# Optimization experiments

Hardware: AMD Instinct MI355X
Metric: run time of the kernel (lower is better)

Reference implementation:

```python
import jax, jax.numpy as jnp
import numpy as np

N_NODES = 100000
N_EDGES = 1600000
N_GRAPHS = 64
HIDDEN = 128


def _gcn_conv(x, W, b, src, dst, norm, n_nodes):
    # PyG GCNConv: out_i = sum_{j->i} norm_ij * (x_j W) + b, with self-loops
    h = x @ W                                   # [N, out]
    msg = h[src] * norm[:, None]                # gather over edges (incl. self-loops)
    out = jax.ops.segment_sum(msg, dst, num_segments=n_nodes)
    return out + b


def _gcn_norm(src, dst, n_nodes):
    # add self-loops, symmetric normalization deg^-1/2 * deg^-1/2
    loops = jnp.arange(n_nodes, dtype=src.dtype)
    src_f = jnp.concatenate([src, loops])
    dst_f = jnp.concatenate([dst, loops])
    deg = jax.ops.segment_sum(jnp.ones_like(dst_f, dtype=jnp.float32), dst_f,
                              num_segments=n_nodes)
    dis = jnp.where(deg > 0, jax.lax.rsqrt(deg), 0.0)
    norm = dis[src_f] * dis[dst_f]
    return src_f, dst_f, norm


def setup_inputs() -> dict:
    key = jax.random.key(0)
    ks = jax.random.split(key, 8)
    x = jax.random.normal(ks[0], (N_NODES, 10), dtype=jnp.float32)
    edge_index = jax.random.randint(ks[1], (2, N_EDGES), 0, N_NODES, dtype=jnp.int64)
    batch = jnp.sort(jax.random.randint(ks[2], (N_NODES,), 0, N_GRAPHS, dtype=jnp.int64))
    g = lambda k, shape: jax.random.normal(k, shape, dtype=jnp.float32) * (1.0 / np.sqrt(shape[0]))
    return {
        "x": x, "edge_index": edge_index, "batch": batch,
        "W1": g(ks[3], (10, HIDDEN)), "b1": jnp.zeros((HIDDEN,), jnp.float32),
        "W2": g(ks[4], (HIDDEN, HIDDEN)), "b2": jnp.zeros((HIDDEN,), jnp.float32),
        "W3": g(ks[5], (HIDDEN, HIDDEN)), "b3": jnp.zeros((HIDDEN,), jnp.float32),
        "Wlin": g(ks[6], (HIDDEN, 3)), "blin": jnp.zeros((3,), jnp.float32),
    }


def reference(x, edge_index, batch, W1, b1, W2, b2, W3, b3, Wlin, blin):
    n = x.shape[0]
    src, dst, norm = _gcn_norm(edge_index[0], edge_index[1], n)
    h = jax.nn.relu(_gcn_conv(x, W1, b1, src, dst, norm, n))
    h = jax.nn.relu(_gcn_conv(h, W2, b2, src, dst, norm, n))
    h = _gcn_conv(h, W3, b3, src, dst, norm, n)
    # global mean pool over graphs
    sums = jax.ops.segment_sum(h, batch, num_segments=N_GRAPHS)
    cnts = jax.ops.segment_sum(jnp.ones((n,), jnp.float32), batch, num_segments=N_GRAPHS)
    pooled = sums / jnp.maximum(cnts, 1.0)[:, None]
    # dropout p=0.5 is identity at eval time
    return pooled @ Wlin + blin
```

## Files before the change

kernel.cpp:

```cpp
#include <hip/hip_runtime.h>

constexpr int NN = 100000;
constexpr int NE = 1600000;
constexpr int NG = 64;
constexpr int H  = 128;

constexpr int NB  = 392;
constexpr int CAP = 5120;
constexpr int P1B = 256;
constexpr int EPB = NE / P1B;

typedef float v2f   __attribute__((ext_vector_type(2)));
typedef float f32x4 __attribute__((ext_vector_type(4)));
typedef short short8 __attribute__((ext_vector_type(8)));

__device__ __forceinline__ float bf_lo(unsigned v) { return __uint_as_float(v << 16); }
__device__ __forceinline__ float bf_hi(unsigned v) { return __uint_as_float(v & 0xffff0000u); }
__device__ __forceinline__ unsigned bf_pack(float a, float b) {
  unsigned ua = __float_as_uint(a);
  unsigned ub = __float_as_uint(b);
  ua += 0x7fffu + ((ua >> 16) & 1u);
  ub += 0x7fffu + ((ub >> 16) & 1u);
  return (ua >> 16) | (ub & 0xffff0000u);
}
__device__ __forceinline__ ushort bf1(float a) {
  unsigned u = __float_as_uint(a);
  u += 0x7fffu + ((u >> 16) & 1u);
  return (ushort)(u >> 16);
}

__device__ __forceinline__ float swap32(float v) {
  int idx = (((int)threadIdx.x & 63) ^ 32) << 2;
  return __int_as_float(__builtin_amdgcn_ds_bpermute(idx, __float_as_int(v)));
}

__global__ void k_init(float* pool, float* cnt, int* gcursor) {
  int i = blockIdx.x * blockDim.x + threadIdx.x;
  if (i < NG * H) pool[i] = 0.f;
  if (i < NG) cnt[i] = 0.f;
  if (i < NB) gcursor[i] = i * CAP;
}

__global__ void k_bucket(const int* __restrict__ ei, int* __restrict__ gcursor,
                         unsigned* __restrict__ ebuf, int* __restrict__ dirs,
                         ushort* __restrict__ dirl) {
  __shared__ int cnt[NB];
  __shared__ int cpos[NB];
  int t = threadIdx.x, b = blockIdx.x;
  for (int j = t; j < NB; j += 256) cnt[j] = 0;
  __syncthreads();
  int e0 = b * EPB;
  for (int i = t; i < EPB; i += 256) {
    int d = ei[NE + e0 + i];
    atomicAdd(&cnt[d >> 8], 1);
  }
  __syncthreads();
  for (int j = t; j < NB; j += 256) {
    int c = cnt[j];
    int start = atomicAdd(&gcursor[j], c);
    cpos[j] = start;
    dirs[b * NB + j] = start;
    dirl[b * NB + j] = (ushort)c;
  }
  __syncthreads();
  for (int j = t; j < NB; j += 256) cnt[j] = 0;
  __syncthreads();
  for (int i = t; i < EPB; i += 256) {
    int s = ei[e0 + i];
    int d = ei[NE + e0 + i];
    int bk = d >> 8;
    int slot = cpos[bk] + atomicAdd(&cnt[bk], 1);
    ebuf[slot] = (unsigned)s | ((unsigned)(d & 255) << 17);
  }
}

__global__ void k_bucketscan(const int* __restrict__ gcursor, int* __restrict__ gbase,
                             int* __restrict__ offs) {
  if (threadIdx.x == 0) {
    int run = 0;
    for (int j = 0; j < NB; ++j) {
      int tot = gcursor[j] - j * CAP;
      gbase[j] = run; run += tot;
    }
    gbase[NB] = run;
    offs[NN] = run;
  }
}

__global__ void k_csr(const unsigned* __restrict__ ebuf, const int* __restrict__ dirs,
                      const ushort* __restrict__ dirl, const int* __restrict__ gbase,
                      const float* __restrict__ x,
                      int* __restrict__ offs, float* __restrict__ dis,
                      unsigned* __restrict__ xs16, int* __restrict__ csr, int n) {
  __shared__ int histc[256];
  __shared__ int loffs[256];
  __shared__ int wps[4];
  int t = threadIdx.x, j = blockIdx.x;
  histc[t] = 0;
  __syncthreads();
  int cstart = dirs[t * NB + j];
  int clen = dirl[t * NB + j];
  for (int k = 0; k < clen; ++k) {
    unsigned u = ebuf[cstart + k];
    atomicAdd(&histc[u >> 17], 1);
  }
  __syncthreads();
  int h = histc[t];
  int inc = h;
  int lane = t & 63;
#pragma unroll
  for (int off = 1; off < 64; off <<= 1) {
    int y = __shfl_up(inc, off, 64);
    if (lane >= off) inc += y;
  }
  if (lane == 63) wps[t >> 6] = inc;
  __syncthreads();
  int woff = 0;
  for (int i = 0; i < (t >> 6); ++i) woff += wps[i];
  int excl = gbase[j] + woff + inc - h;
  loffs[t] = excl;
  int node = j * 256 + t;
  if (node < n) {
    offs[node] = excl;
    float dd = rsqrtf((float)(h + 1));
    dis[node] = dd;
    const float* xr = x + (size_t)node * 10;
#pragma unroll
    for (int q = 0; q < 8; ++q) {
      float a = (2 * q < 10) ? xr[2 * q] * dd : 0.f;
      float bb = (2 * q + 1 < 10) ? xr[2 * q + 1] * dd : 0.f;
      xs16[node * 8 + q] = bf_pack(a, bb);
    }
  }
  __syncthreads();
  for (int k = 0; k < clen; ++k) {
    unsigned u = ebuf[cstart + k];
    int src = (int)(u & 0x1FFFFu);
    int slot = atomicAdd(&loffs[u >> 17], 1);
    csr[slot] = src;
  }
}


__global__ void k_gather16(const int* __restrict__ offs, const int* __restrict__ csr,
                           const float* __restrict__ dis, const unsigned* __restrict__ xs16,
                           float2* __restrict__ agg, int n) {
  int wid = (blockIdx.x * blockDim.x + threadIdx.x) >> 6;
  int lane = threadIdx.x & 63;
  int g = lane >> 3, sl = lane & 7;
  int node = wid * 8 + g;
  if (node >= n) return;
  unsigned self = xs16[node * 8 + sl];
  float sx = bf_lo(self), sy = bf_hi(self);
  float tx = 0.f, ty = 0.f;
  int e = offs[node], end = offs[node + 1];
  for (; e + 3 < end; e += 4) {
    int s0 = csr[e], s1 = csr[e + 1], s2 = csr[e + 2], s3 = csr[e + 3];
    unsigned u0 = xs16[s0 * 8 + sl], u1 = xs16[s1 * 8 + sl];
    unsigned u2 = xs16[s2 * 8 + sl], u3 = xs16[s3 * 8 + sl];
    sx += bf_lo(u0) + bf_lo(u1); tx += bf_lo(u2) + bf_lo(u3);
    sy += bf_hi(u0) + bf_hi(u1); ty += bf_hi(u2) + bf_hi(u3);
  }
  for (; e < end; ++e) {
    unsigned v0 = xs16[csr[e] * 8 + sl];
    sx += bf_lo(v0); sy += bf_hi(v0);
  }
  float dd = dis[node];
  float2 o; o.x = (sx + tx) * dd; o.y = (sy + ty) * dd;
  agg[node * 8 + sl] = o;
}

__global__ void k_mm16(const float* __restrict__ agg, const float* __restrict__ W1,
                       const float* __restrict__ b1, ushort* __restrict__ xbuf, int n) {
  int node = blockIdx.x;
  if (node >= n) return;
  __shared__ float as[16];
  int m = threadIdx.x;
  if (m < 16) as[m] = agg[node * 16 + m];
  __syncthreads();
  float s = 0.f;
#pragma unroll
  for (int k = 0; k < 10; ++k) s += as[k] * W1[k * H + m];
  s += b1[m];
  xbuf[node * H + m] = bf1(fmaxf(s, 0.f));
}

__global__ void k_cvtW2(const float* __restrict__ W2, const float* __restrict__ W3,
                        short* __restrict__ WfragA, short* __restrict__ WfragB) {
  int i = blockIdx.x * blockDim.x + threadIdx.x;
  const float* W = (i < 16384) ? W2 : W3;
  short* outp = (i < 16384) ? WfragA : WfragB;
  int ii = i & 16383;
  int jj = ii & 7, lane = (ii >> 3) & 63, ks = (ii >> 9) & 3, nt = ii >> 11;
  int feat = nt * 16 + (lane & 15);
  int k = ks * 32 + (lane >> 4) * 8 + jj;
  outp[ii] = (short)bf1(W[k * H + feat]);
}

__global__ void k_mm128_mfma(const short* __restrict__ xb,
                             const short* __restrict__ Wfrag,
                             const float* __restrict__ dis,
                             unsigned* __restrict__ hs8, int n) {
  int t = threadIdx.x;
  int lane = t & 63, w = t >> 6;
  int nbase = blockIdx.x * 64 + w * 16;
  int node = nbase + (lane & 15);
  bool valid = node < n;
  int nc = valid ? node : (n - 1);
  short8 xf0, xf1, xf2, xf3;
  const short* xrow = xb + (size_t)nc * H + (lane >> 4) * 8;
  xf0 = *(const short8*)(xrow);
  xf1 = *(const short8*)(xrow + 32);
  xf2 = *(const short8*)(xrow + 64);
  xf3 = *(const short8*)(xrow + 96);
  float d = dis[nc];
  const short8* wf = (const short8*)Wfrag;
#pragma unroll
  for (int nt = 0; nt < 8; ++nt) {
    f32x4 acc = {0.f, 0.f, 0.f, 0.f};
    acc = __builtin_amdgcn_mfma_f32_16x16x32_bf16(wf[(nt * 4 + 0) * 64 + lane], xf0, acc, 0, 0, 0);
    acc = __builtin_amdgcn_mfma_f32_16x16x32_bf16(wf[(nt * 4 + 1) * 64 + lane], xf1, acc, 0, 0, 0);
    acc = __builtin_amdgcn_mfma_f32_16x16x32_bf16(wf[(nt * 4 + 2) * 64 + lane], xf2, acc, 0, 0, 0);
    acc = __builtin_amdgcn_mfma_f32_16x16x32_bf16(wf[(nt * 4 + 3) * 64 + lane], xf3, acc, 0, 0, 0);
    if (valid) {
      int pk = __builtin_amdgcn_cvt_pk_fp8_f32(acc[0] * d, acc[1] * d, 0, false);
      pk = __builtin_amdgcn_cvt_pk_fp8_f32(acc[2] * d, acc[3] * d, pk, true);
      hs8[node * 32 + nt * 4 + (lane >> 4)] = (unsigned)pk;
    }
  }
}

#define RFL(v) __builtin_amdgcn_readfirstlane(v)
#define LOADP(sa, sb) hsu[(size_t)(hihalf ? (sb) : (sa)) * 32 + q]
#define ACCU(uu) { \
    v2f lo_ = __builtin_amdgcn_cvt_pk_f32_fp8((int)(uu), false); \
    v2f hi_ = __builtin_amdgcn_cvt_pk_f32_fp8((int)(uu), true);  \
    a0 += lo_.x; a1 += lo_.y; a2 += hi_.x; a3 += hi_.y; }

template <bool RELU, bool BIAS, bool OUTBF>
__global__ void k_gather(const int* __restrict__ offs, const int* __restrict__ csr,
                         const float* __restrict__ dis, const unsigned* __restrict__ hsu,
                         const float* __restrict__ b, void* __restrict__ outp, int n) {
  int node = (blockIdx.x * blockDim.x + threadIdx.x) >> 6;
  node = RFL(node);
  int lane = threadIdx.x & 63;
  int q = lane & 31;
  bool hihalf = lane >= 32;
  if (node >= n) return;
  float a0 = 0.f, a1 = 0.f, a2 = 0.f, a3 = 0.f;
  float mhi = hihalf ? 0.f : 1.f;
  int e = RFL(offs[node]);
  int end = RFL(offs[node + 1]);

  {
    bool haveB = e < end;
    int sB = haveB ? RFL(csr[e]) : node;
    unsigned u = LOADP(node, sB);
    v2f lo = __builtin_amdgcn_cvt_pk_f32_fp8((int)u, false);
    v2f hi = __builtin_amdgcn_cvt_pk_f32_fp8((int)u, true);
    if (haveB) {
      a0 += lo.x; a1 += lo.y; a2 += hi.x; a3 += hi.y;
      ++e;
    } else {
      a0 += lo.x * mhi; a1 += lo.y * mhi; a2 += hi.x * mhi; a3 += hi.y * mhi;
    }
  }

  for (; e + 15 < end; e += 16) {
    int s0 = RFL(csr[e]),      s1 = RFL(csr[e + 1]);
    int s2 = RFL(csr[e + 2]),  s3 = RFL(csr[e + 3]);
    int s4 = RFL(csr[e + 4]),  s5 = RFL(csr[e + 5]);
    int s6 = RFL(csr[e + 6]),  s7 = RFL(csr[e + 7]);
    int s8 = RFL(csr[e + 8]),  s9 = RFL(csr[e + 9]);
    int sA = RFL(csr[e + 10]), sB = RFL(csr[e + 11]);
    int sC = RFL(csr[e + 12]), sD = RFL(csr[e + 13]);
    int sE = RFL(csr[e + 14]), sF = RFL(csr[e + 15]);
    unsigned u0 = LOADP(s0, s1);
    unsigned u1 = LOADP(s2, s3);
    unsigned u2 = LOADP(s4, s5);
    unsigned u3 = LOADP(s6, s7);
    unsigned u4 = LOADP(s8, s9);
    unsigned u5 = LOADP(sA, sB);
    unsigned u6 = LOADP(sC, sD);
    unsigned u7 = LOADP(sE, sF);
    ACCU(u0); ACCU(u1); ACCU(u2); ACCU(u3);
    ACCU(u4); ACCU(u5); ACCU(u6); ACCU(u7);
  }
  if (e + 7 < end) {
    int s0 = RFL(csr[e]),     s1 = RFL(csr[e + 1]);
    int s2 = RFL(csr[e + 2]), s3 = RFL(csr[e + 3]);
    int s4 = RFL(csr[e + 4]), s5 = RFL(csr[e + 5]);
    int s6 = RFL(csr[e + 6]), s7 = RFL(csr[e + 7]);
    unsigned u0 = LOADP(s0, s1);
    unsigned u1 = LOADP(s2, s3);
    unsigned u2 = LOADP(s4, s5);
    unsigned u3 = LOADP(s6, s7);
    ACCU(u0); ACCU(u1); ACCU(u2); ACCU(u3);
    e += 8;
  }
  if (e + 3 < end) {
    int s0 = RFL(csr[e]),     s1 = RFL(csr[e + 1]);
    int s2 = RFL(csr[e + 2]), s3 = RFL(csr[e + 3]);
    unsigned u0 = LOADP(s0, s1);
    unsigned u1 = LOADP(s2, s3);
    ACCU(u0); ACCU(u1);
    e += 4;
  }
  if (e + 1 < end) {
    int s0 = RFL(csr[e]), s1 = RFL(csr[e + 1]);
    unsigned u0 = LOADP(s0, s1);
    ACCU(u0);
    e += 2;
  }
  if (e < end) {
    int s0 = RFL(csr[e]);
    unsigned u = hsu[(size_t)s0 * 32 + q];
    v2f lo = __builtin_amdgcn_cvt_pk_f32_fp8((int)u, false);
    v2f hi = __builtin_amdgcn_cvt_pk_f32_fp8((int)u, true);
    a0 += lo.x * mhi; a1 += lo.y * mhi; a2 += hi.x * mhi; a3 += hi.y * mhi;
  }

  a0 += swap32(a0);
  a1 += swap32(a1);
  a2 += swap32(a2);
  a3 += swap32(a3);

  if (!hihalf) {
    float dd = dis[node];
    float v0 = a0 * dd, v1 = a1 * dd, v2 = a2 * dd, v3 = a3 * dd;
    if (BIAS) {
      float4 bb = ((const float4*)b)[q];
      v0 += bb.x; v1 += bb.y; v2 += bb.z; v3 += bb.w;
    }
    if (RELU) {
      v0 = fmaxf(v0, 0.f); v1 = fmaxf(v1, 0.f);
      v2 = fmaxf(v2, 0.f); v3 = fmaxf(v3, 0.f);
    }
    if (OUTBF) {
      uint2 o;
      o.x = bf_pack(v0, v1);
      o.y = bf_pack(v2, v3);
      ((uint2*)outp)[(size_t)node * 32 + q] = o;
    } else {
      float4 o; o.x = v0; o.y = v1; o.z = v2; o.w = v3;
      ((float4*)outp)[(size_t)node * 32 + q] = o;
    }
  }
}


__global__ void k_pool(const ushort* __restrict__ acc, const float* __restrict__ b3,
                       const int* __restrict__ batch, float* pool, float* cnt, int n) {
  int m = threadIdx.x;
  int n0 = blockIdx.x * 64;
  float run = 0.f, crun = 0.f;
  int curg = -1;
  float bm = b3[m];
  for (int i = 0; i < 64; ++i) {
    int node = n0 + i;
    if (node >= n) break;
    int g = batch[node];
    if (g != curg) {
      if (curg >= 0) {
        atomicAdd(&pool[curg * H + m], run);
        if (m == 0) atomicAdd(&cnt[curg], crun);
      }
      curg = g; run = 0.f; crun = 0.f;
    }
    run += __uint_as_float((unsigned)acc[node * H + m] << 16) + bm;
    crun += 1.f;
  }
  if (curg >= 0) {
    atomicAdd(&pool[curg * H + m], run);
    if (m == 0) atomicAdd(&cnt[curg], crun);
  }
}

__global__ void k_out(const float* __restrict__ pool, const float* __restrict__ cnt,
                      const float* __restrict__ Wlin, const float* __restrict__ blin,
                      float* __restrict__ out) {
  int t = threadIdx.x;
  if (t >= NG * 3) return;
  int g = t / 3, c = t % 3;
  float invc = 1.f / fmaxf(cnt[g], 1.f);
  float s = 0.f;
  for (int m = 0; m < H; ++m) s += pool[g * H + m] * Wlin[m * 3 + c];
  out[t] = s * invc + blin[c];
}

extern "C" void kernel_launch(void* const* d_in, const int* in_sizes, int n_in,
                              void* d_out, int out_size, void* d_ws, size_t ws_size,
                              hipStream_t stream) {
  const float* x     = (const float*)d_in[0];
  const int*   ei    = (const int*)d_in[1];
  const int*   batch = (const int*)d_in[2];
  const float* W1    = (const float*)d_in[3];
  const float* b1    = (const float*)d_in[4];
  const float* W2    = (const float*)d_in[5];
  const float* b2    = (const float*)d_in[6];
  const float* W3    = (const float*)d_in[7];
  const float* b3    = (const float*)d_in[8];
  const float* Wlin  = (const float*)d_in[9];
  const float* blin  = (const float*)d_in[10];
  float* out = (float*)d_out;

  char* ws = (char*)d_ws;
  float*    dis    = (float*)ws;     ws += sizeof(float) * NN;
  unsigned* hs8    = (unsigned*)ws;  ws += (size_t)NN * H;
  ushort*   xbuf   = (ushort*)ws;    ws += sizeof(ushort) * (size_t)NN * H;
  short*    WfragA = (short*)ws;     ws += sizeof(short) * 16384;
  short*    WfragB = (short*)ws;     ws += sizeof(short) * 16384;
  unsigned* xs16   = (unsigned*)ws;  ws += sizeof(unsigned) * (size_t)NN * 8;
  float*    agg    = (float*)ws;     ws += sizeof(float) * (size_t)NN * 16;
  float*    pool   = (float*)ws;     ws += sizeof(float) * NG * H;
  float*    cnt    = (float*)ws;     ws += sizeof(float) * NG;
  int*      offs   = (int*)ws;       ws += sizeof(int) * (NN + 8);
  int*      csr    = (int*)ws;       ws += sizeof(int) * NE;
  unsigned* ebuf   = (unsigned*)ws;  ws += sizeof(unsigned) * (size_t)NB * CAP;
  int*      dirs   = (int*)ws;       ws += sizeof(int) * P1B * NB;
  ushort*   dirl   = (ushort*)ws;    ws += sizeof(ushort) * P1B * NB;
  int*      gcur   = (int*)ws;       ws += sizeof(int) * NB;
  int*      gbase  = (int*)ws;       ws += sizeof(int) * (NB + 1);

  k_init<<<32, 256, 0, stream>>>(pool, cnt, gcur);
  k_bucket<<<P1B, 256, 0, stream>>>(ei, gcur, ebuf, dirs, dirl);
  k_bucketscan<<<1, 64, 0, stream>>>(gcur, gbase, offs);
  k_csr<<<NB, 256, 0, stream>>>(ebuf, dirs, dirl, gbase, x, offs, dis, xs16, csr, NN);
  k_cvtW2<<<128, 256, 0, stream>>>(W2, W3, WfragA, WfragB);

  const int GATHER_GRID = (NN + 3) / 4;
  const int MM_GRID = (NN + 63) / 64;

  k_gather16<<<(NN + 31) / 32, 256, 0, stream>>>(offs, csr, dis, xs16, (float2*)agg, NN);
  k_mm16<<<NN, 128, 0, stream>>>(agg, W1, b1, xbuf, NN);

  k_mm128_mfma<<<MM_GRID, 256, 0, stream>>>((const short*)xbuf, WfragA, dis, hs8, NN);
  k_gather<true, true, true><<<GATHER_GRID, 256, 0, stream>>>(
      offs, csr, dis, hs8, b2, xbuf, NN);

  k_mm128_mfma<<<MM_GRID, 256, 0, stream>>>((const short*)xbuf, WfragB, dis, hs8, NN);
  k_gather<false, false, true><<<GATHER_GRID, 256, 0, stream>>>(
      offs, csr, dis, hs8, nullptr, xbuf, NN);

  k_pool<<<(NN + 63) / 64, 128, 0, stream>>>(xbuf, b3, batch, pool, cnt, NN);
  k_out<<<1, 256, 0, stream>>>(pool, cnt, Wlin, blin, out);
}
```

Measured before the change: 263.4 us.

## Fuse weight conversion into init, parallelize bucket scan, stage CSR buckets in LDS

Merges the W2/W3 bf16 fragment conversion into the init kernel, removing one launch. The bucket-offset scan moves from a serial single-thread loop to a wave-shuffle scan over 512 threads. k_bucket now reads edges as int2 pairs, and k_csr copies each bucket into shared memory so both histogram passes read LDS instead of global memory twice. k_mm16 now processes 16 nodes per block with W1 held in registers instead of launching one block per node; the 20 KB of LDS per block in k_csr may reduce occupancy.

```diff
diff --git a/kernel.cpp b/kernel.cpp
--- a/kernel.cpp
+++ b/kernel.cpp
@@ -34,11 +34,20 @@
   return __int_as_float(__builtin_amdgcn_ds_bpermute(idx, __float_as_int(v)));
 }
 
-__global__ void k_init(float* pool, float* cnt, int* gcursor) {
+__global__ void k_cvtinit(const float* __restrict__ W2, const float* __restrict__ W3,
+                          short* __restrict__ WfragA, short* __restrict__ WfragB,
+                          float* pool, float* cnt, int* gcursor) {
   int i = blockIdx.x * blockDim.x + threadIdx.x;
   if (i < NG * H) pool[i] = 0.f;
   if (i < NG) cnt[i] = 0.f;
   if (i < NB) gcursor[i] = i * CAP;
+  const float* W = (i < 16384) ? W2 : W3;
+  short* outp = (i < 16384) ? WfragA : WfragB;
+  int ii = i & 16383;
+  int jj = ii & 7, lane = (ii >> 3) & 63, ks = (ii >> 9) & 3, nt = ii >> 11;
+  int feat = nt * 16 + (lane & 15);
+  int k = ks * 32 + (lane >> 4) * 8 + jj;
+  outp[ii] = (short)bf1(W[k * H + feat]);
 }
 
 __global__ void k_bucket(const int* __restrict__ ei, int* __restrict__ gcursor,
@@ -50,9 +59,12 @@
   for (int j = t; j < NB; j += 256) cnt[j] = 0;
   __syncthreads();
   int e0 = b * EPB;
-  for (int i = t; i < EPB; i += 256) {
-    int d = ei[NE + e0 + i];
-    atomicAdd(&cnt[d >> 8], 1);
+  const int2* d2 = (const int2*)&ei[NE + e0];
+  const int2* s2 = (const int2*)&ei[e0];
+  for (int i2 = t; i2 < EPB / 2; i2 += 256) {
+    int2 dv = d2[i2];
+    atomicAdd(&cnt[dv.x >> 8], 1);
+    atomicAdd(&cnt[dv.y >> 8], 1);
   }
   __syncthreads();
   for (int j = t; j < NB; j += 256) {
@@ -65,44 +77,59 @@
   __syncthreads();
   for (int j = t; j < NB; j += 256) cnt[j] = 0;
   __syncthreads();
-  for (int i = t; i < EPB; i += 256) {
-    int s = ei[e0 + i];
-    int d = ei[NE + e0 + i];
-    int bk = d >> 8;
-    int slot = cpos[bk] + atomicAdd(&cnt[bk], 1);
-    ebuf[slot] = (unsigned)s | ((unsigned)(d & 255) << 17);
+  for (int i2 = t; i2 < EPB / 2; i2 += 256) {
+    int2 sv = s2[i2];
+    int2 dv = d2[i2];
+    int bk0 = dv.x >> 8;
+    int slot0 = cpos[bk0] + atomicAdd(&cnt[bk0], 1);
+    ebuf[slot0] = (unsigned)sv.x | ((unsigned)(dv.x & 255) << 17);
+    int bk1 = dv.y >> 8;
+    int slot1 = cpos[bk1] + atomicAdd(&cnt[bk1], 1);
+    ebuf[slot1] = (unsigned)sv.y | ((unsigned)(dv.y & 255) << 17);
   }
 }
 
 __global__ void k_bucketscan(const int* __restrict__ gcursor, int* __restrict__ gbase,
                              int* __restrict__ offs) {
-  if (threadIdx.x == 0) {
-    int run = 0;
-    for (int j = 0; j < NB; ++j) {
-      int tot = gcursor[j] - j * CAP;
-      gbase[j] = run; run += tot;
-    }
-    gbase[NB] = run;
-    offs[NN] = run;
+  __shared__ int ws[8];
+  int t = threadIdx.x;
+  int v = (t < NB) ? (gcursor[t] - t * CAP) : 0;
+  int lane = t & 63, w = t >> 6;
+  int inc = v;
+#pragma unroll
+  for (int off = 1; off < 64; off <<= 1) {
+    int y = __shfl_up(inc, off, 64);
+    if (lane >= off) inc += y;
+  }
+  if (lane == 63) ws[w] = inc;
+  __syncthreads();
+  int woff = 0;
+  for (int i = 0; i < w; ++i) woff += ws[i];
+  if (t < NB) gbase[t] = woff + inc - v;
+  if (t == NB - 1) {
+    gbase[NB] = woff + inc;
+    offs[NN] = woff + inc;
   }
 }
 
 __global__ void k_csr(const unsigned* __restrict__ ebuf, const int* __restrict__ dirs,
                       const ushort* __restrict__ dirl, const int* __restrict__ gbase,
-                      const float* __restrict__ x,
+                      const int* __restrict__ gcur, const float* __restrict__ x,
                       int* __restrict__ offs, float* __restrict__ dis,
                       unsigned* __restrict__ xs16, int* __restrict__ csr, int n) {
+  __shared__ unsigned sh[CAP];
   __shared__ int histc[256];
   __shared__ int loffs[256];
   __shared__ int wps[4];
   int t = threadIdx.x, j = blockIdx.x;
+  int used = gcur[j] - j * CAP;
+  for (int k = t; k < used; k += 256) sh[k] = ebuf[j * CAP + k];
   histc[t] = 0;
   __syncthreads();
-  int cstart = dirs[t * NB + j];
+  int rel = dirs[t * NB + j] - j * CAP;
   int clen = dirl[t * NB + j];
   for (int k = 0; k < clen; ++k) {
-    unsigned u = ebuf[cstart + k];
-    atomicAdd(&histc[u >> 17], 1);
+    atomicAdd(&histc[sh[rel + k] >> 17], 1);
   }
   __syncthreads();
   int h = histc[t];
@@ -134,7 +161,7 @@
   }
   __syncthreads();
   for (int k = 0; k < clen; ++k) {
-    unsigned u = ebuf[cstart + k];
+    unsigned u = sh[rel + k];
     int src = (int)(u & 0x1FFFFu);
     int slot = atomicAdd(&loffs[u >> 17], 1);
     csr[slot] = src;
@@ -172,29 +199,33 @@
 
 __global__ void k_mm16(const float* __restrict__ agg, const float* __restrict__ W1,
                        const float* __restrict__ b1, ushort* __restrict__ xbuf, int n) {
-  int node = blockIdx.x;
-  if (node >= n) return;
-  __shared__ float as[16];
-  int m = threadIdx.x;
-  if (m < 16) as[m] = agg[node * 16 + m];
-  __syncthreads();
-  float s = 0.f;
+  __shared__ float as[16][16];
+  int t = threadIdx.x;
+  int n0 = blockIdx.x * 16;
+  int lnode = t >> 4;
+  int node = n0 + lnode;
+  float v = (node < n) ? agg[(size_t)node * 16 + (t & 15)] : 0.f;
+  as[lnode][t & 15] = v;
+  __syncthreads();
+  int m = t & 127;
+  int half = t >> 7;
+  float w0 = W1[0 * H + m], w1 = W1[1 * H + m], w2 = W1[2 * H + m];
+  float w3 = W1[3 * H + m], w4 = W1[4 * H + m], w5 = W1[5 * H + m];
+  float w6 = W1[6 * H + m], w7 = W1[7 * H + m], w8 = W1[8 * H + m];
+  float w9 = W1[9 * H + m];
+  float bm = b1[m];
 #pragma unroll
-  for (int k = 0; k < 10; ++k) s += as[k] * W1[k * H + m];
-  s += b1[m];
-  xbuf[node * H + m] = bf1(fmaxf(s, 0.f));
-}
-
-__global__ void k_cvtW2(const float* __restrict__ W2, const float* __restrict__ W3,
-                        short* __restrict__ WfragA, short* __restrict__ WfragB) {
-  int i = blockIdx.x * blockDim.x + threadIdx.x;
-  const float* W = (i < 16384) ? W2 : W3;
-  short* outp = (i < 16384) ? WfragA : WfragB;
-  int ii = i & 16383;
-  int jj = ii & 7, lane = (ii >> 3) & 63, ks = (ii >> 9) & 3, nt = ii >> 11;
-  int feat = nt * 16 + (lane & 15);
-  int k = ks * 32 + (lane >> 4) * 8 + jj;
-  outp[ii] = (short)bf1(W[k * H + feat]);
+  for (int j = 0; j < 8; ++j) {
+    int nl = half * 8 + j;
+    int nd = n0 + nl;
+    if (nd < n) {
+      float s = bm;
+      s += as[nl][0] * w0 + as[nl][1] * w1 + as[nl][2] * w2 + as[nl][3] * w3;
+      s += as[nl][4] * w4 + as[nl][5] * w5 + as[nl][6] * w6 + as[nl][7] * w7;
+      s += as[nl][8] * w8 + as[nl][9] * w9;
+      xbuf[(size_t)nd * H + m] = bf1(fmaxf(s, 0.f));
+    }
+  }
 }
 
 __global__ void k_mm128_mfma(const short* __restrict__ xb,
@@ -422,17 +453,16 @@
   int*      gcur   = (int*)ws;       ws += sizeof(int) * NB;
   int*      gbase  = (int*)ws;       ws += sizeof(int) * (NB + 1);
 
-  k_init<<<32, 256, 0, stream>>>(pool, cnt, gcur);
+  k_cvtinit<<<128, 256, 0, stream>>>(W2, W3, WfragA, WfragB, pool, cnt, gcur);
   k_bucket<<<P1B, 256, 0, stream>>>(ei, gcur, ebuf, dirs, dirl);
-  k_bucketscan<<<1, 64, 0, stream>>>(gcur, gbase, offs);
-  k_csr<<<NB, 256, 0, stream>>>(ebuf, dirs, dirl, gbase, x, offs, dis, xs16, csr, NN);
-  k_cvtW2<<<128, 256, 0, stream>>>(W2, W3, WfragA, WfragB);
+  k_bucketscan<<<1, 512, 0, stream>>>(gcur, gbase, offs);
+  k_csr<<<NB, 256, 0, stream>>>(ebuf, dirs, dirl, gbase, gcur, x, offs, dis, xs16, csr, NN);
 
   const int GATHER_GRID = (NN + 3) / 4;
   const int MM_GRID = (NN + 63) / 64;
 
   k_gather16<<<(NN + 31) / 32, 256, 0, stream>>>(offs, csr, dis, xs16, (float2*)agg, NN);
-  k_mm16<<<NN, 128, 0, stream>>>(agg, W1, b1, xbuf, NN);
+  k_mm16<<<(NN + 15) / 16, 256, 0, stream>>>(agg, W1, b1, xbuf, NN);
 
   k_mm128_mfma<<<MM_GRID, 256, 0, stream>>>((const short*)xbuf, WfragA, dis, hs8, NN);
   k_gather<true, true, true><<<GATHER_GRID, 256, 0, stream>>>(
```

Result: faster. 230.9 us (-12.3%).
